# Kernel optimization log

Measured on AMD Instinct MI355X. Metric: run time of the kernel, lower is better.

## Reference

```python
import jax, jax.numpy as jnp
import numpy as np

B, SQ, SK, DIM, HEADS, DH = 2, 1024, 1024, 512, 1, 64
INNER = HEADS * DH  # 64


def setup_inputs() -> dict:
    key = jax.random.key(0)
    ks = jax.random.split(key, 7)
    s = 0.05
    return {
        "x": jax.random.normal(ks[0], (B, SQ, DIM), jnp.float32),
        "emb": jax.random.normal(ks[1], (B, SK, DIM), jnp.float32),
        "Wq": jax.random.normal(ks[2], (DIM, INNER), jnp.float32) * s,
        "Wk": jax.random.normal(ks[3], (DIM, INNER), jnp.float32) * s,
        "Wv": jax.random.normal(ks[4], (DIM, INNER), jnp.float32) * s,
        "Wo": jax.random.normal(ks[5], (INNER, DIM), jnp.float32) * s,
        "bo": jnp.zeros((DIM,), jnp.float32),
    }


def reference(x, emb, Wq, Wk, Wv, Wo, bo):
    # QKV projections (bias-free Dense layers)
    q = x @ Wq     # [B, SQ, INNER]
    k = emb @ Wk   # [B, SK, INNER]
    v = emb @ Wv   # [B, SK, INNER]
    # Faithful to the module's reshape: (B, -1, inner_dim, heads).
    # With heads=1 the attention sees num_heads=INNER and q_features=heads=1.
    q = q.reshape(q.shape[0], -1, q.shape[-1], HEADS)  # [B, SQ, INNER, 1]
    k = k.reshape(k.shape[0], -1, k.shape[-1], HEADS)  # [B, SK, INNER, 1]
    v = v.reshape(v.shape[0], -1, v.shape[-1], HEADS)  # [B, SK, INNER, 1]
    # Memory-efficient attention scales q by q_features**-0.5 (here =1)
    scale = jnp.asarray(q.shape[-1], q.dtype) ** -0.5
    s = jnp.einsum('bqhd,bkhd->bqhk', q * scale, k)    # [B, SQ, INNER, SK]
    p = jax.nn.softmax(s, axis=-1)
    o = jnp.einsum('bqhk,bkhd->bqhd', p, v)            # [B, SQ, INNER, 1]
    o = o.reshape(x.shape[0], x.shape[1], -1)          # [B, SQ, INNER]
    return o @ Wo + bo                                 # [B, SQ, DIM]
```

## Files before the change

kernel.cpp:

```cpp
#include <hip/hip_runtime.h>
#include <hip/hip_bf16.h>

#define LOG2E 1.44269504088896340736f

__device__ __forceinline__ float fast_exp2(float x) {
#if __has_builtin(__builtin_amdgcn_exp2f)
    return __builtin_amdgcn_exp2f(x);
#else
    return exp2f(x);
#endif
}

typedef float f32x2 __attribute__((ext_vector_type(2)));

__device__ __forceinline__ f32x2 pk_fma(f32x2 a, f32x2 b, f32x2 c) {
#if __has_builtin(__builtin_elementwise_fma)
    return __builtin_elementwise_fma(a, b, c);
#else
    f32x2 r; r.x = fmaf(a.x, b.x, c.x); r.y = fmaf(a.y, b.y, c.y); return r;
#endif
}

__global__ __launch_bounds__(256) void proj_kernel(
    const float* __restrict__ x, const float* __restrict__ emb,
    const float* __restrict__ Wq, const float* __restrict__ Wk,
    const float* __restrict__ Wv,
    float* __restrict__ qT, float* __restrict__ kT, float* __restrict__ vT)
{
    __shared__ __align__(16) float sx[4096];
    __shared__ __align__(16) float sred[4096];
    const int t   = threadIdx.x;
    const int bid = blockIdx.x;
    const bool isQ = (bid < 256);
    const int rb  = isQ ? bid : (bid - 256);

    const float* src = (isQ ? x : emb) + (size_t)rb * 8 * 512;
    #pragma unroll
    for (int i = 0; i < 16; ++i) sx[i * 256 + t] = src[i * 256 + t];
    __syncthreads();

    const int b  = rb >> 7;
    const int q0 = (rb << 3) & 1023;

    if (isQ) {
        const int cp = (t & 31) * 2;
        const int g  = t >> 5;
        const int d0 = g * 64;
        f32x2 acc[8];
        #pragma unroll
        for (int r = 0; r < 8; ++r) acc[r] = (f32x2){0.f, 0.f};
        for (int dd = 0; dd < 64; dd += 4) {
            const int d = d0 + dd;
            float2 w0 = *(const float2*)&Wq[(d + 0) * 64 + cp];
            float2 w1 = *(const float2*)&Wq[(d + 1) * 64 + cp];
            float2 w2 = *(const float2*)&Wq[(d + 2) * 64 + cp];
            float2 w3 = *(const float2*)&Wq[(d + 3) * 64 + cp];
            f32x2 w0p = {w0.x, w0.y}, w1p = {w1.x, w1.y};
            f32x2 w2p = {w2.x, w2.y}, w3p = {w3.x, w3.y};
            #pragma unroll
            for (int r = 0; r < 8; ++r) {
                float4 xv = *(const float4*)&sx[r * 512 + d];
                acc[r] = pk_fma((f32x2){xv.x, xv.x}, w0p, acc[r]);
                acc[r] = pk_fma((f32x2){xv.y, xv.y}, w1p, acc[r]);
                acc[r] = pk_fma((f32x2){xv.z, xv.z}, w2p, acc[r]);
                acc[r] = pk_fma((f32x2){xv.w, xv.w}, w3p, acc[r]);
            }
        }
        #pragma unroll
        for (int r = 0; r < 8; ++r)
            *(float2*)&sred[g * 512 + r * 64 + cp] = make_float2(acc[r].x, acc[r].y);
        __syncthreads();
        #pragma unroll
        for (int p = 0; p < 2; ++p) {
            int idx = p * 256 + t;
            int r = idx >> 6, h = idx & 63;
            float s = 0.f;
            #pragma unroll
            for (int g2 = 0; g2 < 8; ++g2) s += sred[g2 * 512 + r * 64 + h];
            qT[(size_t)(b * 64 + h) * 1024 + q0 + r] = s;
        }
    } else {
        const int cp = (t & 63) * 2;
        const int g  = t >> 6;
        const int d0 = g * 128;
        const float* Wsel = (cp < 64) ? (Wk + cp) : (Wv + (cp - 64));
        f32x2 acc[8];
        #pragma unroll
        for (int r = 0; r < 8; ++r) acc[r] = (f32x2){0.f, 0.f};
        for (int dd = 0; dd < 128; dd += 4) {
            const int d = d0 + dd;
            float2 w0 = *(const float2*)&Wsel[(d + 0) * 64];
            float2 w1 = *(const float2*)&Wsel[(d + 1) * 64];
            float2 w2 = *(const float2*)&Wsel[(d + 2) * 64];
            float2 w3 = *(const float2*)&Wsel[(d + 3) * 64];
            f32x2 w0p = {w0.x, w0.y}, w1p = {w1.x, w1.y};
            f32x2 w2p = {w2.x, w2.y}, w3p = {w3.x, w3.y};
            #pragma unroll
            for (int r = 0; r < 8; ++r) {
                float4 xv = *(const float4*)&sx[r * 512 + d];
                acc[r] = pk_fma((f32x2){xv.x, xv.x}, w0p, acc[r]);
                acc[r] = pk_fma((f32x2){xv.y, xv.y}, w1p, acc[r]);
                acc[r] = pk_fma((f32x2){xv.z, xv.z}, w2p, acc[r]);
                acc[r] = pk_fma((f32x2){xv.w, xv.w}, w3p, acc[r]);
            }
        }
        #pragma unroll
        for (int r = 0; r < 8; ++r)
            *(float2*)&sred[g * 1024 + r * 128 + cp] = make_float2(acc[r].x, acc[r].y);
        __syncthreads();
        #pragma unroll
        for (int p = 0; p < 4; ++p) {
            int idx = p * 256 + t;
            int r = idx >> 7, c = idx & 127;
            float s = 0.f;
            #pragma unroll
            for (int g2 = 0; g2 < 4; ++g2) s += sred[g2 * 1024 + r * 128 + c];
            if (c < 64) kT[(size_t)(b * 64 + c) * 1024 + q0 + r] = s;
            else        vT[(size_t)(b * 64 + (c - 64)) * 1024 + q0 + r] = s;
        }
    }
}

__global__ __launch_bounds__(256) void attn_kernel(
    const float* __restrict__ qT, const float* __restrict__ kT,
    const float* __restrict__ vT, float* __restrict__ numP,
    float* __restrict__ denP)
{
    __shared__ __align__(16) float kc[128];
    __shared__ __align__(16) float vc[128];
    __shared__ float wred[8];
    const int t   = threadIdx.x;
    const int bid = blockIdx.x;
    const int b   = bid >> 9;
    const int h   = (bid >> 3) & 63;
    const int je  = bid & 7;
    const size_t base = (size_t)(b * 64 + h) * 1024;

    float kmx = -1e30f, kmn = 1e30f;
    #pragma unroll
    for (int i = 0; i < 4; ++i) {
        float kv = kT[base + i * 256 + t];
        kmx = fmaxf(kmx, kv);
        kmn = fminf(kmn, kv);
    }
    if (t < 128) {
        kc[t] = kT[base + je * 128 + t];
        vc[t] = vT[base + je * 128 + t];
    }
    #pragma unroll
    for (int off = 32; off >= 1; off >>= 1) {
        kmx = fmaxf(kmx, __shfl_xor(kmx, off));
        kmn = fminf(kmn, __shfl_xor(kmn, off));
    }
    const int wid = t >> 6;
    if ((t & 63) == 0) { wred[wid] = kmx; wred[4 + wid] = kmn; }
    __syncthreads();
    kmx = fmaxf(fmaxf(wred[0], wred[1]), fmaxf(wred[2], wred[3]));
    kmn = fminf(fminf(wred[4], wred[5]), fminf(wred[6], wred[7]));

    f32x2 a2[4], b2[4];
    #pragma unroll
    for (int iq = 0; iq < 4; ++iq) {
        const float qs = qT[base + iq * 256 + t];
        const float m  = (qs >= 0.f) ? qs * kmx : qs * kmn;
        const float a  = qs * LOG2E;
        const float bb = -m * LOG2E;
        a2[iq] = (f32x2){a, a};
        b2[iq] = (f32x2){bb, bb};
    }

    f32x2 d01[4], d23[4], n01[4], n23[4];
    #pragma unroll
    for (int iq = 0; iq < 4; ++iq) {
        d01[iq] = (f32x2){0.f, 0.f}; d23[iq] = (f32x2){0.f, 0.f};
        n01[iq] = (f32x2){0.f, 0.f}; n23[iq] = (f32x2){0.f, 0.f};
    }
    const float4* kc4 = (const float4*)kc;
    const float4* vc4 = (const float4*)vc;
    for (int j = 0; j < 32; ++j) {
        float4 k4 = kc4[j];
        float4 v4 = vc4[j];
        f32x2 k01 = {k4.x, k4.y}, k23 = {k4.z, k4.w};
        f32x2 v01 = {v4.x, v4.y}, v23 = {v4.z, v4.w};
        #pragma unroll
        for (int iq = 0; iq < 4; ++iq) {
            f32x2 arg01 = pk_fma(a2[iq], k01, b2[iq]);
            f32x2 arg23 = pk_fma(a2[iq], k23, b2[iq]);
            f32x2 e01, e23;
            e01.x = fast_exp2(arg01.x); e01.y = fast_exp2(arg01.y);
            e23.x = fast_exp2(arg23.x); e23.y = fast_exp2(arg23.y);
            d01[iq] += e01;
            d23[iq] += e23;
            n01[iq] = pk_fma(e01, v01, n01[iq]);
            n23[iq] = pk_fma(e23, v23, n23[iq]);
        }
    }
    #pragma unroll
    for (int iq = 0; iq < 4; ++iq) {
        const float den = (d01[iq].x + d01[iq].y) + (d23[iq].x + d23[iq].y);
        const float num = (n01[iq].x + n01[iq].y) + (n23[iq].x + n23[iq].y);
        const int q = iq * 256 + t;
        const size_t p = (size_t)je * 131072 + (size_t)(b * 1024 + q) * 64 + h;
        numP[p] = num;
        denP[p] = den;
    }
}

__global__ __launch_bounds__(256) void oproj_kernel(
    const float* __restrict__ numP, const float* __restrict__ denP,
    const float* __restrict__ Wo, const float* __restrict__ bo,
    float* __restrict__ out)
{
    __shared__ __align__(16) float so[512];
    const int t  = threadIdx.x;
    const int rb = blockIdx.x;
    const size_t r0 = (size_t)rb * 8;
    #pragma unroll
    for (int p = 0; p < 2; ++p) {
        const size_t gi = r0 * 64 + p * 256 + t;
        float n = 0.f, d = 0.f;
        #pragma unroll
        for (int jp = 0; jp < 8; ++jp) {
            n += numP[gi + (size_t)jp * 131072];
            d += denP[gi + (size_t)jp * 131072];
        }
        so[p * 256 + t] = n / d;
    }
    __syncthreads();

    const int d2 = t * 2;
    float2 bv = *(const float2*)&bo[d2];
    f32x2 acc[8];
    #pragma unroll
    for (int r = 0; r < 8; ++r) acc[r] = (f32x2){bv.x, bv.y};
    for (int hh = 0; hh < 64; hh += 4) {
        float2 w0 = *(const float2*)&Wo[(hh + 0) * 512 + d2];
        float2 w1 = *(const float2*)&Wo[(hh + 1) * 512 + d2];
        float2 w2 = *(const float2*)&Wo[(hh + 2) * 512 + d2];
        float2 w3 = *(const float2*)&Wo[(hh + 3) * 512 + d2];
        f32x2 w0p = {w0.x, w0.y}, w1p = {w1.x, w1.y};
        f32x2 w2p = {w2.x, w2.y}, w3p = {w3.x, w3.y};
        #pragma unroll
        for (int r = 0; r < 8; ++r) {
            float4 s4 = *(const float4*)&so[r * 64 + hh];
            acc[r] = pk_fma((f32x2){s4.x, s4.x}, w0p, acc[r]);
            acc[r] = pk_fma((f32x2){s4.y, s4.y}, w1p, acc[r]);
            acc[r] = pk_fma((f32x2){s4.z, s4.z}, w2p, acc[r]);
            acc[r] = pk_fma((f32x2){s4.w, s4.w}, w3p, acc[r]);
        }
    }
    #pragma unroll
    for (int r = 0; r < 8; ++r)
        *(float2*)&out[(r0 + r) * 512 + d2] = make_float2(acc[r].x, acc[r].y);
}

extern "C" void kernel_launch(void* const* d_in, const int* in_sizes, int n_in,
                              void* d_out, int out_size, void* d_ws, size_t ws_size,
                              hipStream_t stream)
{
    const float* x   = (const float*)d_in[0];
    const float* emb = (const float*)d_in[1];
    const float* Wq  = (const float*)d_in[2];
    const float* Wk  = (const float*)d_in[3];
    const float* Wv  = (const float*)d_in[4];
    const float* Wo  = (const float*)d_in[5];
    const float* bo  = (const float*)d_in[6];
    float* out = (float*)d_out;

    float* qT   = (float*)d_ws;
    float* kT   = qT + 131072;
    float* vT   = kT + 131072;
    float* numP = vT + 131072;
    float* denP = numP + 8 * 131072;

    proj_kernel<<<512, 256, 0, stream>>>(x, emb, Wq, Wk, Wv, qT, kT, vT);
    attn_kernel<<<1024, 256, 0, stream>>>(qT, kT, vT, numP, denP);
    oproj_kernel<<<256, 256, 0, stream>>>(numP, denP, Wo, bo, out);
}
```

Measured before the change: 112.6 us.

## Hoist key min/max into separate kernel and re-split attention work over 2048 blocks

Per-head key max/min is now computed once by a small kernel instead of redundantly in every attention block. The attention kernel changes from 8 key chunks by 4 queries per thread to 4 key chunks of 256 by 1 query per thread, across 2048 blocks with a higher occupancy hint. The partial buffers shrink from 8 to 4 splits, which lowers partial-sum traffic in the output projection. In exchange it adds an extra kernel launch and gives up the per-thread reuse of each shared-memory k/v load across four queries.

```diff
diff --git a/kernel.cpp b/kernel.cpp
--- a/kernel.cpp
+++ b/kernel.cpp
@@ -121,31 +121,18 @@
     }
 }
 
-__global__ __launch_bounds__(256) void attn_kernel(
-    const float* __restrict__ qT, const float* __restrict__ kT,
-    const float* __restrict__ vT, float* __restrict__ numP,
-    float* __restrict__ denP)
-{
-    __shared__ __align__(16) float kc[128];
-    __shared__ __align__(16) float vc[128];
+__global__ __launch_bounds__(256) void kminmax_kernel(
+    const float* __restrict__ kT, float* __restrict__ kmm)
+{
     __shared__ float wred[8];
-    const int t   = threadIdx.x;
-    const int bid = blockIdx.x;
-    const int b   = bid >> 9;
-    const int h   = (bid >> 3) & 63;
-    const int je  = bid & 7;
-    const size_t base = (size_t)(b * 64 + h) * 1024;
-
+    const int t  = threadIdx.x;
+    const int bh = blockIdx.x;
     float kmx = -1e30f, kmn = 1e30f;
     #pragma unroll
     for (int i = 0; i < 4; ++i) {
-        float kv = kT[base + i * 256 + t];
+        float kv = kT[(size_t)bh * 1024 + i * 256 + t];
         kmx = fmaxf(kmx, kv);
         kmn = fminf(kmn, kv);
-    }
-    if (t < 128) {
-        kc[t] = kT[base + je * 128 + t];
-        vc[t] = vT[base + je * 128 + t];
     }
     #pragma unroll
     for (int off = 32; off >= 1; off >>= 1) {
@@ -155,55 +142,67 @@
     const int wid = t >> 6;
     if ((t & 63) == 0) { wred[wid] = kmx; wred[4 + wid] = kmn; }
     __syncthreads();
-    kmx = fmaxf(fmaxf(wred[0], wred[1]), fmaxf(wred[2], wred[3]));
-    kmn = fminf(fminf(wred[4], wred[5]), fminf(wred[6], wred[7]));
-
-    f32x2 a2[4], b2[4];
-    #pragma unroll
-    for (int iq = 0; iq < 4; ++iq) {
-        const float qs = qT[base + iq * 256 + t];
-        const float m  = (qs >= 0.f) ? qs * kmx : qs * kmn;
-        const float a  = qs * LOG2E;
-        const float bb = -m * LOG2E;
-        a2[iq] = (f32x2){a, a};
-        b2[iq] = (f32x2){bb, bb};
-    }
-
-    f32x2 d01[4], d23[4], n01[4], n23[4];
-    #pragma unroll
-    for (int iq = 0; iq < 4; ++iq) {
-        d01[iq] = (f32x2){0.f, 0.f}; d23[iq] = (f32x2){0.f, 0.f};
-        n01[iq] = (f32x2){0.f, 0.f}; n23[iq] = (f32x2){0.f, 0.f};
-    }
+    if (t == 0) {
+        kmx = fmaxf(fmaxf(wred[0], wred[1]), fmaxf(wred[2], wred[3]));
+        kmn = fminf(fminf(wred[4], wred[5]), fminf(wred[6], wred[7]));
+        kmm[bh * 2]     = kmx;
+        kmm[bh * 2 + 1] = kmn;
+    }
+}
+
+__global__ __launch_bounds__(256, 8) void attn_kernel(
+    const float* __restrict__ qT, const float* __restrict__ kT,
+    const float* __restrict__ vT, const float* __restrict__ kmm,
+    float* __restrict__ numP, float* __restrict__ denP)
+{
+    __shared__ __align__(16) float kc[256];
+    __shared__ __align__(16) float vc[256];
+    const int t   = threadIdx.x;
+    const int bid = blockIdx.x;
+    const int b   = bid >> 10;
+    const int h   = (bid >> 4) & 63;
+    const int qq  = (bid >> 2) & 3;
+    const int jq  = bid & 3;
+    const size_t base = (size_t)(b * 64 + h) * 1024;
+
+    kc[t] = kT[base + jq * 256 + t];
+    vc[t] = vT[base + jq * 256 + t];
+    const float kmx = kmm[(b * 64 + h) * 2];
+    const float kmn = kmm[(b * 64 + h) * 2 + 1];
+    __syncthreads();
+
+    const int q = qq * 256 + t;
+    const float qs = qT[base + q];
+    const float m  = (qs >= 0.f) ? qs * kmx : qs * kmn;
+    const float a  = qs * LOG2E;
+    const float bb = -m * LOG2E;
+    const f32x2 a2 = { a, a };
+    const f32x2 b2 = { bb, bb };
+
+    f32x2 d01 = { 0.f, 0.f }, d23 = { 0.f, 0.f };
+    f32x2 n01 = { 0.f, 0.f }, n23 = { 0.f, 0.f };
     const float4* kc4 = (const float4*)kc;
     const float4* vc4 = (const float4*)vc;
-    for (int j = 0; j < 32; ++j) {
+    for (int j = 0; j < 64; ++j) {
         float4 k4 = kc4[j];
         float4 v4 = vc4[j];
-        f32x2 k01 = {k4.x, k4.y}, k23 = {k4.z, k4.w};
-        f32x2 v01 = {v4.x, v4.y}, v23 = {v4.z, v4.w};
-        #pragma unroll
-        for (int iq = 0; iq < 4; ++iq) {
-            f32x2 arg01 = pk_fma(a2[iq], k01, b2[iq]);
-            f32x2 arg23 = pk_fma(a2[iq], k23, b2[iq]);
-            f32x2 e01, e23;
-            e01.x = fast_exp2(arg01.x); e01.y = fast_exp2(arg01.y);
-            e23.x = fast_exp2(arg23.x); e23.y = fast_exp2(arg23.y);
-            d01[iq] += e01;
-            d23[iq] += e23;
-            n01[iq] = pk_fma(e01, v01, n01[iq]);
-            n23[iq] = pk_fma(e23, v23, n23[iq]);
-        }
-    }
-    #pragma unroll
-    for (int iq = 0; iq < 4; ++iq) {
-        const float den = (d01[iq].x + d01[iq].y) + (d23[iq].x + d23[iq].y);
-        const float num = (n01[iq].x + n01[iq].y) + (n23[iq].x + n23[iq].y);
-        const int q = iq * 256 + t;
-        const size_t p = (size_t)je * 131072 + (size_t)(b * 1024 + q) * 64 + h;
-        numP[p] = num;
-        denP[p] = den;
-    }
+        f32x2 k01 = { k4.x, k4.y }, k23 = { k4.z, k4.w };
+        f32x2 v01 = { v4.x, v4.y }, v23 = { v4.z, v4.w };
+        f32x2 arg01 = pk_fma(a2, k01, b2);
+        f32x2 arg23 = pk_fma(a2, k23, b2);
+        f32x2 e01, e23;
+        e01.x = fast_exp2(arg01.x); e01.y = fast_exp2(arg01.y);
+        e23.x = fast_exp2(arg23.x); e23.y = fast_exp2(arg23.y);
+        d01 += e01;
+        d23 += e23;
+        n01 = pk_fma(e01, v01, n01);
+        n23 = pk_fma(e23, v23, n23);
+    }
+    const float den = (d01.x + d01.y) + (d23.x + d23.y);
+    const float num = (n01.x + n01.y) + (n23.x + n23.y);
+    const size_t p = (size_t)jq * 131072 + (size_t)(b * 1024 + q) * 64 + h;
+    numP[p] = num;
+    denP[p] = den;
 }
 
 __global__ __launch_bounds__(256) void oproj_kernel(
@@ -220,7 +219,7 @@
         const size_t gi = r0 * 64 + p * 256 + t;
         float n = 0.f, d = 0.f;
         #pragma unroll
-        for (int jp = 0; jp < 8; ++jp) {
+        for (int jp = 0; jp < 4; ++jp) {
             n += numP[gi + (size_t)jp * 131072];
             d += denP[gi + (size_t)jp * 131072];
         }
@@ -271,9 +270,11 @@
     float* kT   = qT + 131072;
     float* vT   = kT + 131072;
     float* numP = vT + 131072;
-    float* denP = numP + 8 * 131072;
+    float* denP = numP + 4 * 131072;
+    float* kmm  = denP + 4 * 131072;
 
     proj_kernel<<<512, 256, 0, stream>>>(x, emb, Wq, Wk, Wv, qT, kT, vT);
-    attn_kernel<<<1024, 256, 0, stream>>>(qT, kT, vT, numP, denP);
+    kminmax_kernel<<<128, 256, 0, stream>>>(kT, kmm);
+    attn_kernel<<<2048, 256, 0, stream>>>(qT, kT, vT, kmm, numP, denP);
     oproj_kernel<<<256, 256, 0, stream>>>(numP, denP, Wo, bo, out);
 }
```

Result: slower. 115.4 us (+2.5%).
